# Kernel tuning notes

Hardware: AMD Instinct MI355X
Metric: run time of the kernel (lower is better)

Reference implementation:

```python
import jax, jax.numpy as jnp
import numpy as np

B, L, HE, HD, E, AP, T = 128, 128, 1024, 1024, 512, 512, 64

def _lstm_cell(x, h, c, W_ih, W_hh, b_ih, b_hh):
    # torch LSTMCell: gates ordered i, f, g, o
    g = x @ W_ih + b_ih + h @ W_hh + b_hh
    i, f, gg, o = jnp.split(g, 4, axis=-1)
    c_new = jax.nn.sigmoid(f) * c + jax.nn.sigmoid(i) * jnp.tanh(gg)
    h_new = jax.nn.sigmoid(o) * jnp.tanh(c_new)
    return h_new, c_new

def setup_inputs() -> dict:
    key = jax.random.key(0)
    ks = jax.random.split(key, 24)
    def rn(k, shape, scale=0.02):
        return jax.random.normal(k, shape, dtype=jnp.float32) * scale
    inp = {
        "enc_hiddens": jax.random.normal(ks[0], (B, L, HE), dtype=jnp.float32),
        "enc_masks": jnp.zeros((B, L), dtype=jnp.int32),
        "h1_0": rn(ks[1], (B, HD), 1.0), "c1_0": rn(ks[2], (B, HD), 1.0),
        "h2_0": rn(ks[3], (B, HD), 1.0), "c2_0": rn(ks[4], (B, HD), 1.0),
        "captions": jax.random.normal(ks[5], (T, B, E), dtype=jnp.float32),
        # attention params
        "att_W": rn(ks[6], (HE, AP)), "att_b": jnp.zeros((AP,), jnp.float32),
        "dhp_W": rn(ks[7], (HD, AP)), "dhp_b": jnp.zeros((AP,), jnp.float32),
        "corr_w": rn(ks[8], (AP,)), "corr_b": jnp.zeros((), jnp.float32),
        "lt_W": rn(ks[9], (HD, HD)), "lt_b": jnp.zeros((HD,), jnp.float32),
        # LSTM cell 1: input E + HE
        "W_ih1": rn(ks[10], (E + HE, 4 * HD)), "W_hh1": rn(ks[11], (HD, 4 * HD)),
        "b_ih1": jnp.zeros((4 * HD,), jnp.float32), "b_hh1": jnp.zeros((4 * HD,), jnp.float32),
        # LSTM cell 2: input HD
        "W_ih2": rn(ks[12], (HD, 4 * HD)), "W_hh2": rn(ks[13], (HD, 4 * HD)),
        "b_ih2": jnp.zeros((4 * HD,), jnp.float32), "b_hh2": jnp.zeros((4 * HD,), jnp.float32),
    }
    return inp

def reference(enc_hiddens, enc_masks, h1_0, c1_0, h2_0, c2_0, captions,
              att_W, att_b, dhp_W, dhp_b, corr_w, corr_b, lt_W, lt_b,
              W_ih1, W_hh1, b_ih1, b_hh1, W_ih2, W_hh2, b_ih2, b_hh2):
    mask = enc_masks.astype(bool)                      # True == masked (pad)
    enc_proj = enc_hiddens @ att_W + att_b             # (B, L, AP)
    h_prev0 = jnp.ones((enc_hiddens.shape[0], HD), dtype=enc_hiddens.dtype) / HE

    def step(carry, x_t):
        h_prev, h1, c1, h2, c2 = carry
        q = h_prev @ dhp_W + dhp_b                     # (B, AP)
        e = jnp.tanh(enc_proj + q[:, None, :]) @ corr_w + corr_b  # (B, L)
        e = jnp.where(mask, -jnp.inf, e)
        alpha = jax.nn.softmax(e, axis=1)
        a_t = jnp.einsum('bl,blh->bh', alpha, enc_hiddens)
        lstm_in = jnp.concatenate([x_t, a_t], axis=1)
        h1n, c1n = _lstm_cell(lstm_in, h1, c1, W_ih1, W_hh1, b_ih1, b_hh1)
        h2n, c2n = _lstm_cell(h1n, h2, c2, W_ih2, W_hh2, b_ih2, b_hh2)
        # note: output uses layer-1 hidden (matches original); dropout is eval/no-op
        out_t = jnp.tanh(h1n @ lt_W + lt_b)
        # num_decoder_layers == 2 -> next h_prev is layer-2 hidden
        return (h2n, h1n, c1n, h2n, c2n), out_t

    _, outputs = jax.lax.scan(step, (h_prev0, h1_0, c1_0, h2_0, c2_0), captions)
    return outputs                                      # (T, B, HD)
```

## Files before the change

kernel.cpp:

```cpp
#include <hip/hip_runtime.h>
#include <cstdint>
#include <cstddef>

#define DEVI __device__ __forceinline__

typedef __attribute__((ext_vector_type(8))) short short8;
typedef __attribute__((ext_vector_type(4))) float floatx4;

DEVI float bf2f(unsigned short u) { union { unsigned int i; float f; } v; v.i = ((unsigned int)u) << 16; return v.f; }
DEVI unsigned short f2bf(float f) {
  union { float f; unsigned int i; } v; v.f = f;
  unsigned int r = v.i + 0x7fffu + ((v.i >> 16) & 1u);
  return (unsigned short)(r >> 16);
}
DEVI float fsig(float x) { return 1.f / (1.f + __expf(-x)); }
DEVI float ftanh(float x) { return 1.f - 2.f / (__expf(2.f * x) + 1.f); }

DEVI unsigned ld32s(const unsigned* p) { return __hip_atomic_load(p, __ATOMIC_RELAXED, __HIP_MEMORY_SCOPE_AGENT); }
DEVI void st32s(unsigned* p, unsigned v) { __hip_atomic_store(p, v, __ATOMIC_RELAXED, __HIP_MEMORY_SCOPE_AGENT); }
DEVI unsigned add32s(unsigned* p, unsigned v) { return __hip_atomic_fetch_add(p, v, __ATOMIC_RELAXED, __HIP_MEMORY_SCOPE_AGENT); }

struct PP {
  const float *c1_0, *c2_0;
  const float *att_b, *dhp_b, *corr_w, *corr_b, *lt_b;
  const float *b_ih1, *b_hh1, *b_ih2, *b_hh2;
  const int* masks;
  float* out;
  unsigned int* SY; float* q0acc;
  const unsigned short* ench; unsigned short* proj; const unsigned short* caps;
  const unsigned short *W1t, *W2t, *dhpWt, *ltWt, *attWt;
  unsigned short* at; unsigned short* h1b; unsigned short* h2b; float* q;
  float *c1ws, *c2ws;
};

DEVI void zero_g(float* g) {
  for (int i = threadIdx.x; i < 128 * 17; i += 1024) g[i] = 0.f;
}

DEVI int swzb(int row, int kb) { return row * 256 + (kb ^ ((row & 7) << 4)); }

template <int NC, typename AL>
DEVI void gemm_lds(float* g, unsigned short (*As)[16384], unsigned short (*Bs)[2048],
                   const unsigned short* Wtile, int ldw, AL al) {
  const int tid = threadIdx.x, wave = tid >> 6, lane = tid & 63;
  const int sr = tid >> 4, sk8 = (tid & 15) << 3;
  const int wA0 = swzb(sr, (tid & 15) << 4);
  const int wA1 = swzb(sr + 64, (tid & 15) << 4);
  const int wB = swzb(sr & 15, (tid & 15) << 4);
  const unsigned short* wrow = Wtile + (size_t)sr * ldw;
  const int m = wave & 7, kh = wave >> 3;
  const int arow = (m << 4) + (lane & 15);
  const int kq = (lane >> 4) << 3;
  const int rA0 = swzb(arow, (kh * 64 + kq) << 1);
  const int rA1 = swzb(arow, (kh * 64 + 32 + kq) << 1);
  const int rB0 = swzb(lane & 15, (kh * 64 + kq) << 1);
  const int rB1 = swzb(lane & 15, (kh * 64 + 32 + kq) << 1);

  short8 aA[2], aB[2], bA, bB;
  floatx4 acc = (floatx4){0.f, 0.f, 0.f, 0.f};

#define LDCHUNK(c, ra, rb)                                        \
  do {                                                            \
    ra[0] = *(const short8*)al(sr, (c)*128 + sk8);                \
    ra[1] = *(const short8*)al(sr + 64, (c)*128 + sk8);           \
    if (tid < 256) rb = *(const short8*)(wrow + (c)*128 + sk8);   \
  } while (0)
#define STCHUNK(b, ra, rb)                                        \
  do {                                                            \
    char* ab_ = (char*)As[b];                                     \
    *(short8*)(ab_ + wA0) = ra[0];                                \
    *(short8*)(ab_ + wA1) = ra[1];                                \
    if (tid < 256) *(short8*)((char*)Bs[b] + wB) = rb;            \
  } while (0)
#define COMPCH(b)                                                 \
  do {                                                            \
    char* ab_ = (char*)As[b];                                     \
    char* bb_ = (char*)Bs[b];                                     \
    short8 x0 = *(const short8*)(ab_ + rA0);                      \
    short8 y0 = *(const short8*)(bb_ + rB0);                      \
    short8 x1 = *(const short8*)(ab_ + rA1);                      \
    short8 y1 = *(const short8*)(bb_ + rB1);                      \
    acc = __builtin_amdgcn_mfma_f32_16x16x32_bf16(x0, y0, acc, 0, 0, 0); \
    acc = __builtin_amdgcn_mfma_f32_16x16x32_bf16(x1, y1, acc, 0, 0, 0); \
  } while (0)

  LDCHUNK(0, aA, bA);
  LDCHUNK(1, aB, bB);
  STCHUNK(0, aA, bA);
  __syncthreads();
#pragma unroll
  for (int c = 0; c < NC; c += 2) {
    if (c + 2 < NC) LDCHUNK(c + 2, aA, bA);
    COMPCH(0);
    STCHUNK(1, aB, bB);
    __syncthreads();
    if (c + 3 < NC) LDCHUNK(c + 3, aB, bB);
    COMPCH(1);
    if (c + 2 < NC) STCHUNK(0, aA, bA);
    __syncthreads();
  }
#undef LDCHUNK
#undef STCHUNK
#undef COMPCH

  const int col = lane & 15, rr = (lane >> 4) << 2;
#pragma unroll
  for (int r = 0; r < 4; ++r)
    atomicAdd(&g[((m << 4) + rr + r) * 17 + col], acc[r]);
}

DEVI int qidx(int a) { return a + (a >> 6); }

__global__ __launch_bounds__(1024, 4) void k1_attn(PP p, int t) {
  __shared__ float g[128 * 17];
  __shared__ unsigned short As[2][16384];
  __shared__ unsigned short Bs[2][2048];
  __shared__ float q_ss[520], corr_ss[520];
  __shared__ float alpha_s[128], e_s[128];
  __shared__ float redv[2];
  const int tid = threadIdx.x, blk = blockIdx.x;
  const int wave = tid >> 6, lane = tid & 63;

  if (blk < 32) {
    if (t >= 1 && t < 64) {
      zero_g(g);
      const unsigned short* h2p = p.h2b + ((((unsigned)t + 1u) & 1u) << 17);
      auto al = [&](int row, int k) -> const unsigned short* {
        return h2p + ((size_t)row << 10) + k;
      };
      gemm_lds<8>(g, As, Bs, p.dhpWt + (size_t)blk * 16 * 1024, 1024, al);
      __syncthreads();
      for (int e = tid; e < 2048; e += 1024) {
        const int b = e >> 4, col = e & 15, n = blk * 16 + col;
        const float qv = g[b * 17 + col] + p.dhp_b[n];
        st32s((unsigned*)(p.q + b * 512 + n), __float_as_uint(qv));
      }
      __builtin_amdgcn_s_waitcnt(0);
    }
    __syncthreads();
    if (tid == 0) add32s(&p.SY[4], 1u);
  } else if (blk < 160) {
    if (t < 64) {
      const int b = blk - 32;
      if (t >= 1) {
        if (tid == 0) {
          while (ld32s(&p.SY[4]) < (unsigned)(32 * (t + 1))) __builtin_amdgcn_s_sleep(1);
        }
        __syncthreads();
        if (tid < 512) q_ss[qidx(tid)] = __uint_as_float(ld32s((const unsigned*)(p.q + b * 512 + tid)));
      } else {
        if (tid < 512) q_ss[qidx(tid)] = p.q[b * 512 + tid];
      }
      if (tid < 512) corr_ss[qidx(tid)] = p.corr_w[tid];
      __syncthreads();
      {
        const int l = tid >> 3, l8 = tid & 7;
        const unsigned short* pp_ = p.proj + ((size_t)(b * 128 + l)) * 512 + l8 * 64;
        short8 vv[8];
#pragma unroll
        for (int j = 0; j < 8; ++j) vv[j] = *(const short8*)(pp_ + j * 8);
        float acc = 0.f;
#pragma unroll
        for (int j = 0; j < 8; ++j)
#pragma unroll
          for (int i = 0; i < 8; ++i) {
            const int ap = l8 * 64 + j * 8 + i;
            acc += ftanh(bf2f((unsigned short)vv[j][i]) + q_ss[qidx(ap)]) * corr_ss[qidx(ap)];
          }
        acc += __shfl_down(acc, 4, 8);
        acc += __shfl_down(acc, 2, 8);
        acc += __shfl_down(acc, 1, 8);
        if (l8 == 0) {
          acc += p.corr_b[0];
          if (p.masks[b * 128 + l] != 0) acc = -1e30f;
          e_s[l] = acc;
        }
      }
      __syncthreads();
      if (wave == 0) {
        float m0 = fmaxf(e_s[lane], e_s[lane + 64]);
#pragma unroll
        for (int off = 32; off; off >>= 1) m0 = fmaxf(m0, __shfl_xor(m0, off));
        const float a0 = __expf(e_s[lane] - m0), a1 = __expf(e_s[lane + 64] - m0);
        alpha_s[lane] = a0; alpha_s[lane + 64] = a1;
        float s = a0 + a1;
#pragma unroll
        for (int off = 32; off; off >>= 1) s += __shfl_xor(s, off);
        if (lane == 0) redv[0] = 1.f / s;
      }
      __syncthreads();
      {
        const float inv = redv[0];
        const unsigned short* pe = p.ench + ((size_t)b << 17) + tid;
        float acc = 0.f;
#pragma unroll 16
        for (int l = 0; l < 128; ++l) acc += alpha_s[l] * bf2f(pe[(size_t)l << 10]);
        p.at[(b << 10) + tid] = f2bf(acc * inv);
      }
    }
  } else {
    if (t >= 1) {
      const int ob = blk - 160, ot = t - 1;
      zero_g(g);
      const unsigned short* h1 = p.h1b + (((unsigned)ot & 1u) << 17);
      auto al = [&](int row, int k) -> const unsigned short* {
        return h1 + ((size_t)row << 10) + k;
      };
      gemm_lds<8>(g, As, Bs, p.ltWt + (size_t)ob * 16 * 1024, 1024, al);
      __syncthreads();
      for (int e = tid; e < 2048; e += 1024) {
        const int b = e >> 4, col = e & 15, n = ob * 16 + col;
        p.out[(size_t)ot * 131072 + (b << 10) + n] = ftanh(g[b * 17 + col] + p.lt_b[n]);
      }
    }
  }
}

__global__ __launch_bounds__(1024, 4) void k2_g1(PP p, int t) {
  __shared__ float g[128 * 17];
  __shared__ unsigned short As[2][16384];
  __shared__ unsigned short Bs[2][2048];
  const int tid = threadIdx.x, blk = blockIdx.x;
  zero_g(g);
  const unsigned short* caps_t = p.caps + ((size_t)t << 16);
  const unsigned short* h1p = p.h1b + ((((unsigned)t + 1u) & 1u) << 17);
  const unsigned short* at_ = p.at;
  auto al = [&](int row, int k) -> const unsigned short* {
    if (k < 512) return caps_t + ((size_t)row << 9) + k;
    if (k < 1536) return at_ + ((size_t)row << 10) + (k - 512);
    return h1p + ((size_t)row << 10) + (k - 1536);
  };
  gemm_lds<20>(g, As, Bs, p.W1t + (size_t)blk * 16 * 2560, 2560, al);
  __syncthreads();
  if (tid < 512) {
    const int b = tid >> 2, c = tid & 3;
    const int cidx = b * 1024 + blk * 4 + c;
    const float cprev = (t == 0) ? p.c1_0[cidx] : p.c1ws[cidx];
    const float gi = g[b * 17 + c]      + p.b_ih1[blk * 4 + c]        + p.b_hh1[blk * 4 + c];
    const float gf = g[b * 17 + 4 + c]  + p.b_ih1[1024 + blk * 4 + c] + p.b_hh1[1024 + blk * 4 + c];
    const float gg = g[b * 17 + 8 + c]  + p.b_ih1[2048 + blk * 4 + c] + p.b_hh1[2048 + blk * 4 + c];
    const float go = g[b * 17 + 12 + c] + p.b_ih1[3072 + blk * 4 + c] + p.b_hh1[3072 + blk * 4 + c];
    const float cn = fsig(gf) * cprev + fsig(gi) * ftanh(gg);
    p.c1ws[cidx] = cn;
    p.h1b[(((unsigned)t & 1u) << 17) + (b << 10) + blk * 4 + c] = f2bf(fsig(go) * ftanh(cn));
  }
}

__global__ __launch_bounds__(1024, 4) void k3_g2(PP p, int t) {
  __shared__ float g[128 * 17];
  __shared__ unsigned short As[2][16384];
  __shared__ unsigned short Bs[2][2048];
  const int tid = threadIdx.x, blk = blockIdx.x;
  zero_g(g);
  const unsigned short* h1c = p.h1b + (((unsigned)t & 1u) << 17);
  const unsigned short* h2p = p.h2b + ((((unsigned)t + 1u) & 1u) << 17);
  auto al = [&](int row, int k) -> const unsigned short* {
    if (k < 1024) return h1c + ((size_t)row << 10) + k;
    return h2p + ((size_t)row << 10) + (k - 1024);
  };
  gemm_lds<16>(g, As, Bs, p.W2t + (size_t)blk * 16 * 2048, 2048, al);
  __syncthreads();
  if (tid < 512) {
    const int b = tid >> 2, c = tid & 3;
    const int cidx = b * 1024 + blk * 4 + c;
    const float cprev = (t == 0) ? p.c2_0[cidx] : p.c2ws[cidx];
    const float gi = g[b * 17 + c]      + p.b_ih2[blk * 4 + c]        + p.b_hh2[blk * 4 + c];
    const float gf = g[b * 17 + 4 + c]  + p.b_ih2[1024 + blk * 4 + c] + p.b_hh2[1024 + blk * 4 + c];
    const float gg = g[b * 17 + 8 + c]  + p.b_ih2[2048 + blk * 4 + c] + p.b_hh2[2048 + blk * 4 + c];
    const float go = g[b * 17 + 12 + c] + p.b_ih2[3072 + blk * 4 + c] + p.b_hh2[3072 + blk * 4 + c];
    const float cn = fsig(gf) * cprev + fsig(gi) * ftanh(gg);
    p.c2ws[cidx] = cn;
    p.h2b[(((unsigned)t & 1u) << 17) + (b << 10) + blk * 4 + c] = f2bf(fsig(go) * ftanh(cn));
  }
}

__global__ __launch_bounds__(512) void k_zero(unsigned int* SY, float* q0) {
  SY[threadIdx.x] = 0u;
  q0[threadIdx.x] = 0.f;
}

__global__ __launch_bounds__(256) void k_cvt(const float* caps, const float* ench,
                                             const float* h1_0, const float* h2_0,
                                             unsigned short* o_caps, unsigned short* o_ench,
                                             unsigned short* o_h1, unsigned short* o_h2) {
  const size_t i = (size_t)blockIdx.x * 256 + threadIdx.x;
  if (i < 4194304u) o_caps[i] = f2bf(caps[i]);
  else if (i < 20971520u) o_ench[i - 4194304u] = f2bf(ench[i - 4194304u]);
  else if (i < 21102592u) o_h1[i - 20971520u] = f2bf(h1_0[i - 20971520u]);
  else o_h2[i - 21102592u] = f2bf(h2_0[i - 21102592u]);
}

__global__ __launch_bounds__(256) void k_tr(const float* srcA, const float* srcB, int ksplit,
                                            int K, int stride, int Nrows, int perm,
                                            unsigned short* out, float* q0) {
  __shared__ float lds[64][5];
  const int nbr = Nrows >> 2;
  const int rt = blockIdx.x % nbr, kt = blockIdx.x / nbr;
  const int r0 = rt * 4, k0 = kt * 64;
  int oc0;
  if (perm) { const int nb = r0 >> 4, gg = (r0 & 15) >> 2; oc0 = gg * 1024 + nb * 4; }
  else oc0 = r0;
  {
    const int kk = threadIdx.x >> 2, rr = threadIdx.x & 3;
    const int k = k0 + kk;
    const float* s = (k < ksplit) ? (srcA + (size_t)k * stride) : (srcB + (size_t)(k - ksplit) * stride);
    lds[kk][rr] = s[oc0 + rr];
  }
  __syncthreads();
  if (q0 != nullptr && threadIdx.x < 4) {
    float t = 0.f;
    for (int kk = 0; kk < 64; ++kk) t += lds[kk][threadIdx.x];
    atomicAdd(&q0[oc0 + threadIdx.x], t);
  }
  {
    const int rr = threadIdx.x >> 6, kk = threadIdx.x & 63;
    out[(size_t)(r0 + rr) * K + k0 + kk] = f2bf(lds[kk][rr]);
  }
}

__global__ __launch_bounds__(1024, 4) void k_proj(PP p) {
  const int tid = threadIdx.x, blk = blockIdx.x;
  const int wave = tid >> 6, lane = tid & 63;
  const int kq = ((lane >> 4) << 3), m16 = lane & 15;
  const int mw = wave & 3, ng = wave >> 2;
  const int mtile = blk * 4 + mw;
  const int mrow = mtile * 16 + m16;
  floatx4 acc[8];
#pragma unroll
  for (int nt = 0; nt < 8; ++nt) acc[nt] = (floatx4){0.f, 0.f, 0.f, 0.f};
  for (int s = 0; s < 32; ++s) {
    const int k = (s << 5) + kq;
    short8 af = *(const short8*)(p.ench + (size_t)mrow * 1024 + k);
#pragma unroll
    for (int nt = 0; nt < 8; ++nt) {
      short8 bf = *(const short8*)(p.attWt + (size_t)(ng * 128 + nt * 16 + m16) * 1024 + k);
      acc[nt] = __builtin_amdgcn_mfma_f32_16x16x32_bf16(af, bf, acc[nt], 0, 0, 0);
    }
  }
#pragma unroll
  for (int nt = 0; nt < 8; ++nt)
#pragma unroll
    for (int r = 0; r < 4; ++r) {
      const int rowg = mtile * 16 + ((lane >> 4) << 2) + r;
      const int col = ng * 128 + nt * 16 + m16;
      p.proj[(size_t)rowg * 512 + col] = f2bf(acc[nt][r] + p.att_b[col]);
    }
}

__global__ __launch_bounds__(1024) void k_qinit(float* q, const float* q0acc, const float* dhp_b) {
  const int i = blockIdx.x * 1024 + threadIdx.x;
  const int n = i & 511;
  q[i] = q0acc[n] * (1.f / 1024.f) + dhp_b[n];
}

extern "C" void kernel_launch(void* const* d_in, const int* in_sizes, int n_in,
                              void* d_out, int out_size, void* d_ws, size_t ws_size,
                              hipStream_t stream) {
  const float* enc_hiddens = (const float*)d_in[0];
  const int*   enc_masks   = (const int*)d_in[1];
  const float* h1_0 = (const float*)d_in[2];
  const float* c1_0 = (const float*)d_in[3];
  const float* h2_0 = (const float*)d_in[4];
  const float* c2_0 = (const float*)d_in[5];
  const float* captions = (const float*)d_in[6];
  const float* att_W = (const float*)d_in[7];
  const float* att_b = (const float*)d_in[8];
  const float* dhp_W = (const float*)d_in[9];
  const float* dhp_b = (const float*)d_in[10];
  const float* corr_w = (const float*)d_in[11];
  const float* corr_b = (const float*)d_in[12];
  const float* lt_W = (const float*)d_in[13];
  const float* lt_b = (const float*)d_in[14];
  const float* W_ih1 = (const float*)d_in[15];
  const float* W_hh1 = (const float*)d_in[16];
  const float* b_ih1 = (const float*)d_in[17];
  const float* b_hh1 = (const float*)d_in[18];
  const float* W_ih2 = (const float*)d_in[19];
  const float* W_hh2 = (const float*)d_in[20];
  const float* b_ih2 = (const float*)d_in[21];
  const float* b_hh2 = (const float*)d_in[22];

  uint8_t* w = (uint8_t*)d_ws;
  unsigned int* SY = (unsigned int*)w;
  float* q0acc = (float*)(w + 2048);
  size_t off = 4096;
  unsigned short* ench  = (unsigned short*)(w + off); off += 33554432;
  unsigned short* proj  = (unsigned short*)(w + off); off += 16777216;
  unsigned short* caps  = (unsigned short*)(w + off); off += 8388608;
  unsigned short* W1t   = (unsigned short*)(w + off); off += 20971520;
  unsigned short* W2t   = (unsigned short*)(w + off); off += 16777216;
  unsigned short* dhpWt = (unsigned short*)(w + off); off += 1048576;
  unsigned short* ltWt  = (unsigned short*)(w + off); off += 2097152;
  unsigned short* attWt = (unsigned short*)(w + off); off += 1048576;
  unsigned short* at_   = (unsigned short*)(w + off); off += 262144;
  unsigned short* h1b   = (unsigned short*)(w + off); off += 524288;
  unsigned short* h2b   = (unsigned short*)(w + off); off += 524288;
  float* qb             = (float*)(w + off);          off += 262144;
  float* c1ws           = (float*)(w + off);          off += 524288;
  float* c2ws           = (float*)(w + off);          off += 524288;
  if (ws_size < off) return;

  k_zero<<<1, 512, 0, stream>>>(SY, q0acc);
  k_cvt<<<82944, 256, 0, stream>>>(captions, enc_hiddens, h1_0, h2_0,
                                   caps, ench, h1b + 131072, h2b + 131072);
  k_tr<<<40960, 256, 0, stream>>>(W_ih1, W_hh1, 1536, 2560, 4096, 4096, 1, W1t, nullptr);
  k_tr<<<32768, 256, 0, stream>>>(W_ih2, W_hh2, 1024, 2048, 4096, 4096, 1, W2t, nullptr);
  k_tr<<<2048, 256, 0, stream>>>(dhp_W, dhp_W, 1024, 1024, 512, 512, 0, dhpWt, q0acc);
  k_tr<<<4096, 256, 0, stream>>>(lt_W, lt_W, 1024, 1024, 1024, 1024, 0, ltWt, nullptr);
  k_tr<<<2048, 256, 0, stream>>>(att_W, att_W, 1024, 1024, 512, 512, 0, attWt, nullptr);
  k_qinit<<<64, 1024, 0, stream>>>(qb, q0acc, dhp_b);

  PP p;
  p.c1_0 = c1_0; p.c2_0 = c2_0;
  p.att_b = att_b; p.dhp_b = dhp_b; p.corr_w = corr_w; p.corr_b = corr_b; p.lt_b = lt_b;
  p.b_ih1 = b_ih1; p.b_hh1 = b_hh1; p.b_ih2 = b_ih2; p.b_hh2 = b_hh2;
  p.masks = enc_masks;
  p.out = (float*)d_out;
  p.SY = SY; p.q0acc = q0acc;
  p.ench = ench; p.proj = proj; p.caps = caps;
  p.W1t = W1t; p.W2t = W2t; p.dhpWt = dhpWt; p.ltWt = ltWt; p.attWt = attWt;
  p.at = at_; p.h1b = h1b; p.h2b = h2b; p.q = qb;
  p.c1ws = c1ws; p.c2ws = c2ws;

  k_proj<<<256, 1024, 0, stream>>>(p);

  for (int t = 0; t < 64; ++t) {
    k1_attn<<<224, 1024, 0, stream>>>(p, t);
    k2_g1<<<256, 1024, 0, stream>>>(p, t);
    k3_g2<<<256, 1024, 0, stream>>>(p, t);
  }
  k1_attn<<<224, 1024, 0, stream>>>(p, 64);
}
```

Baseline: 4.942 ms.

## Tile encoder projection through LDS, vectorize bf16 conversion, lighten GEMM barriers

```diff
diff --git a/kernel.cpp b/kernel.cpp
--- a/kernel.cpp
+++ b/kernel.cpp
@@ -6,6 +6,7 @@
 
 typedef __attribute__((ext_vector_type(8))) short short8;
 typedef __attribute__((ext_vector_type(4))) float floatx4;
+typedef __attribute__((ext_vector_type(4))) unsigned short ushortx4;
 
 DEVI float bf2f(unsigned short u) { union { unsigned int i; float f; } v; v.i = ((unsigned int)u) << 16; return v.f; }
 DEVI unsigned short f2bf(float f) {
@@ -19,6 +20,8 @@
 DEVI unsigned ld32s(const unsigned* p) { return __hip_atomic_load(p, __ATOMIC_RELAXED, __HIP_MEMORY_SCOPE_AGENT); }
 DEVI void st32s(unsigned* p, unsigned v) { __hip_atomic_store(p, v, __ATOMIC_RELAXED, __HIP_MEMORY_SCOPE_AGENT); }
 DEVI unsigned add32s(unsigned* p, unsigned v) { return __hip_atomic_fetch_add(p, v, __ATOMIC_RELAXED, __HIP_MEMORY_SCOPE_AGENT); }
+
+DEVI void bar_nd() { asm volatile("s_waitcnt lgkmcnt(0)\ns_barrier" ::: "memory"); }
 
 struct PP {
   const float *c1_0, *c2_0;
@@ -87,17 +90,17 @@
   LDCHUNK(0, aA, bA);
   LDCHUNK(1, aB, bB);
   STCHUNK(0, aA, bA);
-  __syncthreads();
+  bar_nd();
 #pragma unroll
   for (int c = 0; c < NC; c += 2) {
     if (c + 2 < NC) LDCHUNK(c + 2, aA, bA);
     COMPCH(0);
     STCHUNK(1, aB, bB);
-    __syncthreads();
+    bar_nd();
     if (c + 3 < NC) LDCHUNK(c + 3, aB, bB);
     COMPCH(1);
     if (c + 2 < NC) STCHUNK(0, aA, bA);
-    __syncthreads();
+    bar_nd();
   }
 #undef LDCHUNK
 #undef STCHUNK
@@ -279,15 +282,19 @@
   q0[threadIdx.x] = 0.f;
 }
 
-__global__ __launch_bounds__(256) void k_cvt(const float* caps, const float* ench,
-                                             const float* h1_0, const float* h2_0,
-                                             unsigned short* o_caps, unsigned short* o_ench,
-                                             unsigned short* o_h1, unsigned short* o_h2) {
-  const size_t i = (size_t)blockIdx.x * 256 + threadIdx.x;
-  if (i < 4194304u) o_caps[i] = f2bf(caps[i]);
-  else if (i < 20971520u) o_ench[i - 4194304u] = f2bf(ench[i - 4194304u]);
-  else if (i < 21102592u) o_h1[i - 20971520u] = f2bf(h1_0[i - 20971520u]);
-  else o_h2[i - 21102592u] = f2bf(h2_0[i - 21102592u]);
+__global__ __launch_bounds__(256) void k_cvt4(const float* caps, const float* ench,
+                                              const float* h1_0, const float* h2_0,
+                                              unsigned short* o_caps, unsigned short* o_ench,
+                                              unsigned short* o_h1, unsigned short* o_h2) {
+  const size_t i = ((size_t)blockIdx.x * 256 + threadIdx.x) << 2;
+  const float* s; unsigned short* d; size_t off;
+  if (i < 4194304u) { s = caps; d = o_caps; off = i; }
+  else if (i < 20971520u) { s = ench; d = o_ench; off = i - 4194304u; }
+  else if (i < 21102592u) { s = h1_0; d = o_h1; off = i - 20971520u; }
+  else { s = h2_0; d = o_h2; off = i - 21102592u; }
+  floatx4 v = *(const floatx4*)(s + off);
+  ushortx4 o = { f2bf(v[0]), f2bf(v[1]), f2bf(v[2]), f2bf(v[3]) };
+  *(ushortx4*)(d + off) = o;
 }
 
 __global__ __launch_bounds__(256) void k_tr(const float* srcA, const float* srcB, int ksplit,
@@ -318,33 +325,96 @@
   }
 }
 
-__global__ __launch_bounds__(1024, 4) void k_proj(PP p) {
+__global__ __launch_bounds__(1024, 4) void k_proj2(PP p) {
+  __shared__ unsigned short As[2][16384];
+  __shared__ unsigned short Bs[2][16384];
   const int tid = threadIdx.x, blk = blockIdx.x;
+  const int mb = blk >> 2, nb = blk & 3;
+  const int m0 = mb << 7, n0 = nb << 7;
   const int wave = tid >> 6, lane = tid & 63;
-  const int kq = ((lane >> 4) << 3), m16 = lane & 15;
-  const int mw = wave & 3, ng = wave >> 2;
-  const int mtile = blk * 4 + mw;
-  const int mrow = mtile * 16 + m16;
-  floatx4 acc[8];
-#pragma unroll
-  for (int nt = 0; nt < 8; ++nt) acc[nt] = (floatx4){0.f, 0.f, 0.f, 0.f};
-  for (int s = 0; s < 32; ++s) {
-    const int k = (s << 5) + kq;
-    short8 af = *(const short8*)(p.ench + (size_t)mrow * 1024 + k);
-#pragma unroll
-    for (int nt = 0; nt < 8; ++nt) {
-      short8 bf = *(const short8*)(p.attWt + (size_t)(ng * 128 + nt * 16 + m16) * 1024 + k);
-      acc[nt] = __builtin_amdgcn_mfma_f32_16x16x32_bf16(af, bf, acc[nt], 0, 0, 0);
+  const int sr = tid >> 4, sk8 = (tid & 15) << 3;
+  const int wL0 = swzb(sr, (tid & 15) << 4);
+  const int wL1 = swzb(sr + 64, (tid & 15) << 4);
+  const int mw = wave & 7, nh = wave >> 3;
+  const int m16 = lane & 15, kq = (lane >> 4) << 3;
+  const unsigned short* Ag  = p.ench  + ((size_t)(m0 + sr) << 10);
+  const unsigned short* Ag2 = p.ench  + ((size_t)(m0 + sr + 64) << 10);
+  const unsigned short* Bg  = p.attWt + ((size_t)(n0 + sr) << 10);
+  const unsigned short* Bg2 = p.attWt + ((size_t)(n0 + sr + 64) << 10);
+
+  const int ar = mw * 16 + m16;
+  const int aBase = ar * 256, aX = (ar & 7) << 4;
+  const int bX = (m16 & 7) << 4;
+  int bBase[4];
+#pragma unroll
+  for (int nf = 0; nf < 4; ++nf) bBase[nf] = (nh * 64 + nf * 16 + m16) * 256;
+
+  floatx4 acc[4];
+#pragma unroll
+  for (int nf = 0; nf < 4; ++nf) acc[nf] = (floatx4){0.f, 0.f, 0.f, 0.f};
+
+  short8 xa0, xa1, xb0, xb1, ya0, ya1, yb0, yb1;
+
+#define PJLD(c, r0_, r1_, r2_, r3_)                      \
+  do {                                                   \
+    r0_ = *(const short8*)(Ag + (c) * 128 + sk8);        \
+    r1_ = *(const short8*)(Ag2 + (c) * 128 + sk8);       \
+    r2_ = *(const short8*)(Bg + (c) * 128 + sk8);        \
+    r3_ = *(const short8*)(Bg2 + (c) * 128 + sk8);       \
+  } while (0)
+#define PJST(b, r0_, r1_, r2_, r3_)                      \
+  do {                                                   \
+    *(short8*)((char*)As[b] + wL0) = r0_;                \
+    *(short8*)((char*)As[b] + wL1) = r1_;                \
+    *(short8*)((char*)Bs[b] + wL0) = r2_;                \
+    *(short8*)((char*)Bs[b] + wL1) = r3_;                \
+  } while (0)
+#define PJCOMP(b)                                                        \
+  do {                                                                   \
+    char* ab_ = (char*)As[b];                                            \
+    char* bb_ = (char*)Bs[b];                                            \
+    _Pragma("unroll")                                                    \
+    for (int ks = 0; ks < 4; ++ks) {                                     \
+      const int kb = ks * 64 + (kq << 1);                                \
+      short8 af = *(const short8*)(ab_ + aBase + (kb ^ aX));             \
+      _Pragma("unroll")                                                  \
+      for (int nf = 0; nf < 4; ++nf) {                                   \
+        short8 bf = *(const short8*)(bb_ + bBase[nf] + (kb ^ bX));       \
+        acc[nf] = __builtin_amdgcn_mfma_f32_16x16x32_bf16(af, bf, acc[nf], 0, 0, 0); \
+      }                                                                  \
+    }                                                                    \
+  } while (0)
+
+  PJLD(0, xa0, xa1, xb0, xb1);
+  PJLD(1, ya0, ya1, yb0, yb1);
+  PJST(0, xa0, xa1, xb0, xb1);
+  bar_nd();
+#pragma unroll
+  for (int c = 0; c < 8; c += 2) {
+    if (c + 2 < 8) PJLD(c + 2, xa0, xa1, xb0, xb1);
+    PJCOMP(0);
+    PJST(1, ya0, ya1, yb0, yb1);
+    bar_nd();
+    if (c + 3 < 8) PJLD(c + 3, ya0, ya1, yb0, yb1);
+    PJCOMP(1);
+    if (c + 2 < 8) PJST(0, xa0, xa1, xb0, xb1);
+    bar_nd();
+  }
+#undef PJLD
+#undef PJST
+#undef PJCOMP
+
+  const int r0 = (lane >> 4) << 2;
+#pragma unroll
+  for (int nf = 0; nf < 4; ++nf) {
+    const int col = n0 + nh * 64 + nf * 16 + m16;
+    const float ab = p.att_b[col];
+#pragma unroll
+    for (int r = 0; r < 4; ++r) {
+      const int row = m0 + mw * 16 + r0 + r;
+      p.proj[(size_t)row * 512 + col] = f2bf(acc[nf][r] + ab);
     }
   }
-#pragma unroll
-  for (int nt = 0; nt < 8; ++nt)
-#pragma unroll
-    for (int r = 0; r < 4; ++r) {
-      const int rowg = mtile * 16 + ((lane >> 4) << 2) + r;
-      const int col = ng * 128 + nt * 16 + m16;
-      p.proj[(size_t)rowg * 512 + col] = f2bf(acc[nt][r] + p.att_b[col]);
-    }
 }
 
 __global__ __launch_bounds__(1024) void k_qinit(float* q, const float* q0acc, const float* dhp_b) {
@@ -401,8 +471,8 @@
   if (ws_size < off) return;
 
   k_zero<<<1, 512, 0, stream>>>(SY, q0acc);
-  k_cvt<<<82944, 256, 0, stream>>>(captions, enc_hiddens, h1_0, h2_0,
-                                   caps, ench, h1b + 131072, h2b + 131072);
+  k_cvt4<<<20736, 256, 0, stream>>>(captions, enc_hiddens, h1_0, h2_0,
+                                    caps, ench, h1b + 131072, h2b + 131072);
   k_tr<<<40960, 256, 0, stream>>>(W_ih1, W_hh1, 1536, 2560, 4096, 4096, 1, W1t, nullptr);
   k_tr<<<32768, 256, 0, stream>>>(W_ih2, W_hh2, 1024, 2048, 4096, 4096, 1, W2t, nullptr);
   k_tr<<<2048, 256, 0, stream>>>(dhp_W, dhp_W, 1024, 1024, 512, 512, 0, dhpWt, q0acc);
@@ -422,7 +492,7 @@
   p.at = at_; p.h1b = h1b; p.h2b = h2b; p.q = qb;
   p.c1ws = c1ws; p.c2ws = c2ws;
 
-  k_proj<<<256, 1024, 0, stream>>>(p);
+  k_proj2<<<512, 1024, 0, stream>>>(p);
 
   for (int t = 0; t < 64; ++t) {
     k1_attn<<<224, 1024, 0, stream>>>(p, t);
```

New measurement: 4.831 ms. 2.2% less time.
